# Performance work log

Hardware: AMD Instinct MI355X
Metric: run time of the kernel (lower is better)

The kernel has to match this reference:

```python
import jax, jax.numpy as jnp
import numpy as np

H, KD, VD = 12, 64, 64  # num_heads, k_dim, v_dim
EPS = 1e-12

def _l2norm(x, axis):
    n = jnp.linalg.norm(x, axis=axis, keepdims=True)
    return x / jnp.maximum(n, EPS)

def setup_inputs() -> dict:
    key = jax.random.key(0)
    ks = jax.random.split(key, 6)
    d1, d2 = 768, 768
    return {
        "x1": jax.random.normal(ks[0], (2048, d1), jnp.float32),
        "x2": jax.random.normal(ks[1], (8192, d2), jnp.float32),
        "Wq": jax.random.normal(ks[2], (H * KD, d1), jnp.float32) * 0.03,
        "Wk": jax.random.normal(ks[3], (H * KD, d2), jnp.float32) * 0.03,
        "Wv": jax.random.normal(ks[4], (H * VD, d2), jnp.float32) * 0.03,
        "Wo": jax.random.normal(ks[5], (d1, H * VD), jnp.float32) * 0.03,
        "invt": 20,
    }

def reference(x1, x2, Wq, Wk, Wv, Wo, invt):
    B1 = x1.shape[0]
    B2 = x2.shape[0]
    # Linear (no bias): y = x @ W.T, then split heads
    q = (x1 @ Wq.T).reshape(B1, H, KD)  # [B1,H,KD]
    k = (x2 @ Wk.T).reshape(B2, H, KD)  # [B2,H,KD]
    v = (x2 @ Wv.T).reshape(B2, H, VD)  # [B2,H,VD]
    # per-head L2 normalization over feature dim (cosine attention)
    q = _l2norm(q, axis=-1)
    k = _l2norm(k, axis=-1)
    attn = jnp.einsum("bhd,nhd->hbn", q, k) * jnp.float32(invt)  # [H,B1,B2]
    attn = jax.nn.softmax(attn, axis=-1)
    out = jnp.einsum("hbn,nhd->bhd", attn, v).reshape(B1, H * VD)
    out = out @ Wo.T  # [B1, in_dim1]
    return _l2norm(out, axis=1)
```

## Files before the change

kernel.cpp:

```cpp
#include <hip/hip_runtime.h>
#include <hip/hip_bf16.h>
#include <math.h>

#define B1 2048
#define B2 8192
#define NH 12
#define DH 64
#define DMODEL 768

typedef __attribute__((ext_vector_type(8))) short short8;
typedef __attribute__((ext_vector_type(4))) float floatx4;
typedef __attribute__((ext_vector_type(8))) unsigned short ushort8;
typedef __attribute__((ext_vector_type(4))) unsigned short ushort4v;

static __device__ __forceinline__ unsigned short f2bf(float f) {
  __bf16 b = (__bf16)f;
  return __builtin_bit_cast(unsigned short, b);
}

static __device__ __forceinline__ void gload16(const unsigned short* g,
                                               unsigned short* l) {
  __builtin_amdgcn_global_load_lds(
      (const __attribute__((address_space(1))) void*)g,
      (__attribute__((address_space(3))) void*)l, 16, 0, 0);
}

template <bool L2N, bool F32OUT>
static __device__ __forceinline__ void gemm_tile_f32(
    const float* __restrict__ Ag, const float* __restrict__ Bg,
    void* __restrict__ Cv, int M, int N, int K, int m0, int n0,
    unsigned short* sAh, unsigned short* sBh) {
  const int tid = threadIdx.x;
  const int wave = tid >> 6;
  const int lane = tid & 63;
  const int wm = wave >> 1;
  const int wn = wave & 1;
  const int n15 = lane & 15;
  const int quad = lane >> 4;
  const int srow = lane >> 2;
  const int cpl = (lane & 3) ^ (srow >> 2);

  floatx4 acc[4][4];
#pragma unroll
  for (int i = 0; i < 4; ++i)
#pragma unroll
    for (int j = 0; j < 4; ++j) acc[i][j] = (floatx4){0.f, 0.f, 0.f, 0.f};

  float4 ar[2][2], br[2][2];
#pragma unroll
  for (int jj = 0; jj < 2; ++jj) {
    const int row = (wave * 2 + jj) * 16 + srow;
    const size_t ga = (size_t)(m0 + row) * K + cpl * 8;
    const size_t gb = (size_t)(n0 + row) * K + cpl * 8;
    ar[jj][0] = *(const float4*)&Ag[ga];
    ar[jj][1] = *(const float4*)&Ag[ga + 4];
    br[jj][0] = *(const float4*)&Bg[gb];
    br[jj][1] = *(const float4*)&Bg[gb + 4];
  }

  for (int k0 = 0; k0 < K; k0 += 32) {
    __syncthreads();
#pragma unroll
    for (int jj = 0; jj < 2; ++jj) {
      const int j = wave * 2 + jj;
      const float4 a0 = ar[jj][0], a1 = ar[jj][1];
      const float4 b0 = br[jj][0], b1 = br[jj][1];
      ushort8 ah = {f2bf(a0.x), f2bf(a0.y), f2bf(a0.z), f2bf(a0.w),
                    f2bf(a1.x), f2bf(a1.y), f2bf(a1.z), f2bf(a1.w)};
      ushort8 bh = {f2bf(b0.x), f2bf(b0.y), f2bf(b0.z), f2bf(b0.w),
                    f2bf(b1.x), f2bf(b1.y), f2bf(b1.z), f2bf(b1.w)};
      *(ushort8*)&sAh[j * 512 + lane * 8] = ah;
      *(ushort8*)&sBh[j * 512 + lane * 8] = bh;
    }
    if (k0 + 32 < K) {
#pragma unroll
      for (int jj = 0; jj < 2; ++jj) {
        const int row = (wave * 2 + jj) * 16 + srow;
        const size_t ga = (size_t)(m0 + row) * K + (k0 + 32) + cpl * 8;
        const size_t gb = (size_t)(n0 + row) * K + (k0 + 32) + cpl * 8;
        ar[jj][0] = *(const float4*)&Ag[ga];
        ar[jj][1] = *(const float4*)&Ag[ga + 4];
        br[jj][0] = *(const float4*)&Bg[gb];
        br[jj][1] = *(const float4*)&Bg[gb + 4];
      }
    }
    __syncthreads();

    short8 afh[4];
#pragma unroll
    for (int mt = 0; mt < 4; ++mt) {
      const int row = wm * 64 + mt * 16 + n15;
      const int off = row * 32 + ((quad ^ (n15 >> 2)) << 3);
      afh[mt] = *(const short8*)&sAh[off];
    }
#pragma unroll
    for (int nt = 0; nt < 4; ++nt) {
      const int row = wn * 64 + nt * 16 + n15;
      const int off = row * 32 + ((quad ^ (n15 >> 2)) << 3);
      const short8 bfh = *(const short8*)&sBh[off];
#pragma unroll
      for (int mt = 0; mt < 4; ++mt)
        acc[mt][nt] = __builtin_amdgcn_mfma_f32_16x16x32_bf16(afh[mt], bfh, acc[mt][nt], 0, 0, 0);
    }
  }

#pragma unroll
  for (int mt = 0; mt < 4; ++mt) {
    float scalev[4] = {1.f, 1.f, 1.f, 1.f};
    if constexpr (L2N) {
#pragma unroll
      for (int rr = 0; rr < 4; ++rr) {
        float ss = 0.f;
#pragma unroll
        for (int nt = 0; nt < 4; ++nt) ss += acc[mt][nt][rr] * acc[mt][nt][rr];
        ss += __shfl_xor(ss, 1, 64);
        ss += __shfl_xor(ss, 2, 64);
        ss += __shfl_xor(ss, 4, 64);
        ss += __shfl_xor(ss, 8, 64);
        scalev[rr] = 1.0f / fmaxf(sqrtf(ss), 1e-12f);
      }
    }
#pragma unroll
    for (int nt = 0; nt < 4; ++nt) {
#pragma unroll
      for (int rr = 0; rr < 4; ++rr) {
        const int row = m0 + wm * 64 + mt * 16 + quad * 4 + rr;
        const int col = n0 + wn * 64 + nt * 16 + n15;
        const float v = acc[mt][nt][rr] * scalev[rr];
        if constexpr (F32OUT)
          ((float*)Cv)[(size_t)row * N + col] = v;
        else
          ((unsigned short*)Cv)[(size_t)row * N + col] = f2bf(v);
      }
    }
  }
}

__global__ __launch_bounds__(256) void qkv_proj(
    const float* __restrict__ x1, const float* __restrict__ Wq,
    const float* __restrict__ x2, const float* __restrict__ Wk,
    const float* __restrict__ Wv,
    unsigned short* __restrict__ qbf, unsigned short* __restrict__ kbf,
    unsigned short* __restrict__ vtbf) {
  __shared__ __align__(16) unsigned short sAh[4096], sBh[4096];
  const int bi = blockIdx.x;
  if (bi < 96) {
    gemm_tile_f32<true, false>(x1, Wq, qbf, B1, DMODEL, DMODEL,
                               (bi / 6) * 128, (bi % 6) * 128, sAh, sBh);
  } else if (bi < 480) {
    const int b = bi - 96;
    gemm_tile_f32<true, false>(x2, Wk, kbf, B2, DMODEL, DMODEL,
                               (b / 6) * 128, (b % 6) * 128, sAh, sBh);
  } else {
    const int b = bi - 480;
    gemm_tile_f32<false, false>(Wv, x2, vtbf, DMODEL, B2, DMODEL,
                                (b / 64) * 128, (b % 64) * 128, sAh, sBh);
  }
}

#define KC 128
#define KSPLIT 2
#define NCH (B2 / KSPLIT / KC)
#define PSTR 68

__global__ __launch_bounds__(256, 3) void attn_mfma(
    const unsigned short* __restrict__ qb, const unsigned short* __restrict__ kb,
    const unsigned short* __restrict__ vt, float* __restrict__ aoacc,
    float* __restrict__ lacc, const int* __restrict__ invt_p) {
  __shared__ __align__(16) unsigned short smem[25088];
  unsigned short* Psl = smem + 16384;

  const int bid = blockIdx.x;
  const int swz = (bid & 7) * 96 + (bid >> 3);
  const int zz = swz / 384;
  const int rem = swz - zz * 384;
  const int h = rem >> 5;
  const int q0 = (rem & 31) * 64;

  const float c2 = (float)invt_p[0] * 1.4426950408889634f;
  const int tid = threadIdx.x;
  const int wave = tid >> 6;
  const int lane = tid & 63;
  const int qsub = wave >> 1;
  const int ksub = wave & 1;
  const int n15 = lane & 15;
  const int quad = lane >> 4;
  const int kz0 = zz * (B2 / KSPLIT);

  unsigned short* Ps = &Psl[wave * 32 * PSTR];

  short8 qf[2][2];
#pragma unroll
  for (int qt = 0; qt < 2; ++qt)
#pragma unroll
    for (int ks = 0; ks < 2; ++ks) {
      const int qrow = q0 + qsub * 32 + qt * 16 + n15;
      qf[qt][ks] = *(const short8*)&qb[(size_t)qrow * DMODEL + h * DH + ks * 32 + quad * 8];
    }

  floatx4 oacc[2][4];
#pragma unroll
  for (int qt = 0; qt < 2; ++qt)
#pragma unroll
    for (int nt = 0; nt < 4; ++nt) oacc[qt][nt] = (floatx4){0.f, 0.f, 0.f, 0.f};
  float lsum[2] = {0.f, 0.f};

  const unsigned short* kbp = kb + (size_t)kz0 * DMODEL + h * DH;
  const unsigned short* vbp = vt + (size_t)(h * DH) * B2 + kz0;

  ushort8 kr[4];
#pragma unroll
  for (int i = 0; i < 4; ++i) {
    const int s = i * 256 + tid;
    const int key = s >> 3, cpk = s & 7, chk = cpk ^ (key & 7);
    kr[i] = *(const ushort8*)&kbp[(size_t)key * DMODEL + chk * 8];
  }
#pragma unroll
  for (int i = 0; i < 4; ++i) {
    const int s = i * 256 + tid;
    const int key = s >> 3, cpk = s & 7;
    *(ushort8*)&smem[key * 64 + cpk * 8] = kr[i];
  }
#pragma unroll
  for (int i = 0; i < 4; ++i) {
    const int s = i * 256 + tid;
    const int key = s >> 3, cpk = s & 7, chk = cpk ^ (key & 7);
    kr[i] = *(const ushort8*)&kbp[(size_t)(KC + key) * DMODEL + chk * 8];
  }
  __syncthreads();

  for (int c = 0; c < NCH; ++c) {
    unsigned short* Kb = &smem[(c & 1) * 8192];
    unsigned short* Kn = &smem[((c + 1) & 1) * 8192];
    const unsigned short* vc_ = vbp + c * KC;

    ushort8 vr[8];
#pragma unroll
    for (int ks = 0; ks < 2; ++ks)
#pragma unroll
      for (int nt = 0; nt < 4; ++nt)
        vr[ks * 4 + nt] = *(const ushort8*)&vc_[
            (size_t)(nt * 16 + n15) * B2 + (ksub * 8 + ks * 4 + quad) * 8];

    if (c + 1 < NCH) {
#pragma unroll
      for (int i = 0; i < 4; ++i) {
        const int s = i * 256 + tid;
        const int key = s >> 3, cpk = s & 7;
        *(ushort8*)&Kn[key * 64 + cpk * 8] = kr[i];
      }
      if (c + 2 < NCH) {
        const unsigned short* k2 = kbp + (size_t)(c + 2) * KC * DMODEL;
#pragma unroll
        for (int i = 0; i < 4; ++i) {
          const int s = i * 256 + tid;
          const int key = s >> 3, cpk = s & 7, chk = cpk ^ (key & 7);
          kr[i] = *(const ushort8*)&k2[(size_t)key * DMODEL + chk * 8];
        }
      }
    }

#pragma unroll
    for (int kt = 0; kt < 4; ++kt) {
      floatx4 s0 = {0.f, 0.f, 0.f, 0.f}, s1 = {0.f, 0.f, 0.f, 0.f};
#pragma unroll
      for (int ks = 0; ks < 2; ++ks) {
        const int key = ksub * 64 + kt * 16 + n15;
        const int cp = (ks * 4 + quad) ^ (n15 & 7);
        const short8 kf = *(const short8*)&Kb[key * 64 + cp * 8];
        s0 = __builtin_amdgcn_mfma_f32_16x16x32_bf16(kf, qf[0][ks], s0, 0, 0, 0);
        s1 = __builtin_amdgcn_mfma_f32_16x16x32_bf16(kf, qf[1][ks], s1, 0, 0, 0);
      }
      ushort4v p0, p1;
#pragma unroll
      for (int r = 0; r < 4; ++r) {
        const float e0 = exp2f(fmaf(s0[r], c2, -c2));
        const float e1 = exp2f(fmaf(s1[r], c2, -c2));
        lsum[0] += e0;
        lsum[1] += e1;
        p0[r] = f2bf(e0);
        p1[r] = f2bf(e1);
      }
      *(ushort4v*)&Ps[(0 * 16 + n15) * PSTR + kt * 16 + quad * 4] = p0;
      *(ushort4v*)&Ps[(1 * 16 + n15) * PSTR + kt * 16 + quad * 4] = p1;
    }

#pragma unroll
    for (int ks = 0; ks < 2; ++ks) {
      short8 pa[2];
#pragma unroll
      for (int qt = 0; qt < 2; ++qt)
        pa[qt] = *(const short8*)&Ps[(qt * 16 + n15) * PSTR + ks * 32 + quad * 8];
#pragma unroll
      for (int nt = 0; nt < 4; ++nt) {
        const short8 vf = __builtin_bit_cast(short8, vr[ks * 4 + nt]);
        oacc[0][nt] = __builtin_amdgcn_mfma_f32_16x16x32_bf16(pa[0], vf, oacc[0][nt], 0, 0, 0);
        oacc[1][nt] = __builtin_amdgcn_mfma_f32_16x16x32_bf16(pa[1], vf, oacc[1][nt], 0, 0, 0);
      }
    }

    __syncthreads();
  }

#pragma unroll
  for (int qt = 0; qt < 2; ++qt) {
    float v = lsum[qt];
    v += __shfl_xor(v, 16, 64);
    v += __shfl_xor(v, 32, 64);
    lsum[qt] = v;
  }

  float* aoz = aoacc + (size_t)zz * B1 * DMODEL;
  float* lz = lacc + (size_t)zz * B1 * NH;

  __syncthreads();
  float* Osc = (float*)smem;
  float* lsc = Osc + 4096;
  if (ksub == 1) {
#pragma unroll
    for (int qt = 0; qt < 2; ++qt)
#pragma unroll
      for (int nt = 0; nt < 4; ++nt)
#pragma unroll
        for (int r = 0; r < 4; ++r) {
          const int row = qsub * 32 + qt * 16 + quad * 4 + r;
          Osc[row * 64 + nt * 16 + n15] = oacc[qt][nt][r];
        }
    if (quad == 0) {
      lsc[qsub * 32 + n15] = lsum[0];
      lsc[qsub * 32 + 16 + n15] = lsum[1];
    }
  }
  __syncthreads();
  if (ksub == 0) {
#pragma unroll
    for (int qt = 0; qt < 2; ++qt)
#pragma unroll
      for (int nt = 0; nt < 4; ++nt)
#pragma unroll
        for (int r = 0; r < 4; ++r) {
          const int row = qsub * 32 + qt * 16 + quad * 4 + r;
          const float v = oacc[qt][nt][r] + Osc[row * 64 + nt * 16 + n15];
          aoz[(size_t)(q0 + row) * DMODEL + h * DH + nt * 16 + n15] = v;
        }
    if (quad == 0) {
      lz[(size_t)(q0 + qsub * 32 + n15) * NH + h] = lsum[0] + lsc[qsub * 32 + n15];
      lz[(size_t)(q0 + qsub * 32 + 16 + n15) * NH + h] =
          lsum[1] + lsc[qsub * 32 + 16 + n15];
    }
  }
}

__global__ __launch_bounds__(256) void wo_proj(
    const float* __restrict__ aoacc, const float* __restrict__ lacc,
    const float* __restrict__ Wo, float* __restrict__ woout) {
  __shared__ __align__(16) unsigned short sAh[4096], sBh[4096];
  const int bi = blockIdx.x;
  const int m0 = (bi / 6) * 128;
  const int n0 = (bi % 6) * 128;
  const int tid = threadIdx.x;
  const int wave = tid >> 6;
  const int lane = tid & 63;
  const int wm = wave >> 1;
  const int wn = wave & 1;
  const int n15 = lane & 15;
  const int quad = lane >> 4;
  const int srow = lane >> 2;
  const int cpl = (lane & 3) ^ (srow >> 2);

  const float* ao1 = aoacc + (size_t)B1 * DMODEL;
  const float* la1 = lacc + (size_t)B1 * NH;

  floatx4 acc[4][4];
#pragma unroll
  for (int i = 0; i < 4; ++i)
#pragma unroll
    for (int j = 0; j < 4; ++j) acc[i][j] = (floatx4){0.f, 0.f, 0.f, 0.f};

  for (int k0 = 0; k0 < DMODEL; k0 += 32) {
    __syncthreads();
#pragma unroll
    for (int jj = 0; jj < 2; ++jj) {
      const int j = wave * 2 + jj;
      const int row = j * 16 + srow;
      const size_t ga = (size_t)(m0 + row) * DMODEL + k0 + cpl * 8;
      const float4 a0 = *(const float4*)&aoacc[ga];
      const float4 a1 = *(const float4*)&aoacc[ga + 4];
      const float4 b0 = *(const float4*)&ao1[ga];
      const float4 b1 = *(const float4*)&ao1[ga + 4];
      const int head = (k0 + cpl * 8) >> 6;
      const float lsum = lacc[(m0 + row) * NH + head] + la1[(m0 + row) * NH + head];
      const float inv = 1.0f / lsum;
      ushort8 ah = {f2bf((a0.x + b0.x) * inv), f2bf((a0.y + b0.y) * inv),
                    f2bf((a0.z + b0.z) * inv), f2bf((a0.w + b0.w) * inv),
                    f2bf((a1.x + b1.x) * inv), f2bf((a1.y + b1.y) * inv),
                    f2bf((a1.z + b1.z) * inv), f2bf((a1.w + b1.w) * inv)};
      *(ushort8*)&sAh[j * 512 + lane * 8] = ah;
      const size_t gb = (size_t)(n0 + row) * DMODEL + k0 + cpl * 8;
      const float4 w0 = *(const float4*)&Wo[gb];
      const float4 w1 = *(const float4*)&Wo[gb + 4];
      ushort8 bh = {f2bf(w0.x), f2bf(w0.y), f2bf(w0.z), f2bf(w0.w),
                    f2bf(w1.x), f2bf(w1.y), f2bf(w1.z), f2bf(w1.w)};
      *(ushort8*)&sBh[j * 512 + lane * 8] = bh;
    }
    __syncthreads();

    short8 afh[4];
#pragma unroll
    for (int mt = 0; mt < 4; ++mt) {
      const int row = wm * 64 + mt * 16 + n15;
      afh[mt] = *(const short8*)&sAh[row * 32 + ((quad ^ (n15 >> 2)) << 3)];
    }
#pragma unroll
    for (int nt = 0; nt < 4; ++nt) {
      const int row = wn * 64 + nt * 16 + n15;
      const short8 bfh = *(const short8*)&sBh[row * 32 + ((quad ^ (n15 >> 2)) << 3)];
#pragma unroll
      for (int mt = 0; mt < 4; ++mt)
        acc[mt][nt] = __builtin_amdgcn_mfma_f32_16x16x32_bf16(afh[mt], bfh, acc[mt][nt], 0, 0, 0);
    }
  }

#pragma unroll
  for (int mt = 0; mt < 4; ++mt)
#pragma unroll
    for (int nt = 0; nt < 4; ++nt)
#pragma unroll
      for (int rr = 0; rr < 4; ++rr) {
        const int row = m0 + wm * 64 + mt * 16 + quad * 4 + rr;
        const int col = n0 + wn * 64 + nt * 16 + n15;
        woout[(size_t)row * DMODEL + col] = acc[mt][nt][rr];
      }
}

__global__ __launch_bounds__(256) void l2norm_rows768_out(
    const float* __restrict__ x, float* __restrict__ out) {
  const int row = blockIdx.x;
  const float* xr = &x[(size_t)row * DMODEL];
  float ss = 0.0f;
  float vals[3];
#pragma unroll
  for (int i = 0; i < 3; ++i) {
    vals[i] = xr[threadIdx.x + i * 256];
    ss += vals[i] * vals[i];
  }
#pragma unroll
  for (int off = 32; off > 0; off >>= 1) ss += __shfl_xor(ss, off, 64);
  __shared__ float ws[4];
  if ((threadIdx.x & 63) == 0) ws[threadIdx.x >> 6] = ss;
  __syncthreads();
  const float tot = ws[0] + ws[1] + ws[2] + ws[3];
  const float sc = 1.0f / fmaxf(sqrtf(tot), 1e-12f);
  float* orow = &out[(size_t)row * DMODEL];
#pragma unroll
  for (int i = 0; i < 3; ++i) orow[threadIdx.x + i * 256] = vals[i] * sc;
}

extern "C" void kernel_launch(void* const* d_in, const int* in_sizes, int n_in,
                              void* d_out, int out_size, void* d_ws,
                              size_t ws_size, hipStream_t stream) {
  const float* x1 = (const float*)d_in[0];
  const float* x2 = (const float*)d_in[1];
  const float* Wq = (const float*)d_in[2];
  const float* Wk = (const float*)d_in[3];
  const float* Wv = (const float*)d_in[4];
  const float* Wo = (const float*)d_in[5];
  const int* invt = (const int*)d_in[6];
  float* outp = (float*)d_out;

  char* ws = (char*)d_ws;
  float* aoacc = (float*)(ws + 0);
  float* woout = (float*)(ws + 12582912);
  unsigned short* vt_bf = (unsigned short*)(ws + 18874368);
  float* lacc = (float*)(ws + 32636928);
  unsigned short* q_bf = (unsigned short*)(ws + 38535168);
  unsigned short* k_bf = (unsigned short*)(ws + 41680896);

  qkv_proj<<<864, 256, 0, stream>>>(x1, Wq, x2, Wk, Wv, q_bf, k_bf, vt_bf);
  attn_mfma<<<768, 256, 0, stream>>>(q_bf, k_bf, vt_bf, aoacc, lacc, invt);
  wo_proj<<<96, 256, 0, stream>>>(aoacc, lacc, Wo, woout);
  l2norm_rows768_out<<<B1, 256, 0, stream>>>(woout, outp);
}
```

Measured before the change: 291.1 us.

## Split-K the output projection and double-buffer LDS in the projection GEMMs

```diff
diff --git a/kernel.cpp b/kernel.cpp
--- a/kernel.cpp
+++ b/kernel.cpp
@@ -18,18 +18,11 @@
   return __builtin_bit_cast(unsigned short, b);
 }
 
-static __device__ __forceinline__ void gload16(const unsigned short* g,
-                                               unsigned short* l) {
-  __builtin_amdgcn_global_load_lds(
-      (const __attribute__((address_space(1))) void*)g,
-      (__attribute__((address_space(3))) void*)l, 16, 0, 0);
-}
-
 template <bool L2N, bool F32OUT>
 static __device__ __forceinline__ void gemm_tile_f32(
     const float* __restrict__ Ag, const float* __restrict__ Bg,
     void* __restrict__ Cv, int M, int N, int K, int m0, int n0,
-    unsigned short* sAh, unsigned short* sBh) {
+    unsigned short* sA, unsigned short* sB) {
   const int tid = threadIdx.x;
   const int wave = tid >> 6;
   const int lane = tid & 63;
@@ -39,6 +32,7 @@
   const int quad = lane >> 4;
   const int srow = lane >> 2;
   const int cpl = (lane & 3) ^ (srow >> 2);
+  const int nstep = K >> 5;
 
   floatx4 acc[4][4];
 #pragma unroll
@@ -57,51 +51,77 @@
     br[jj][0] = *(const float4*)&Bg[gb];
     br[jj][1] = *(const float4*)&Bg[gb + 4];
   }
-
-  for (int k0 = 0; k0 < K; k0 += 32) {
-    __syncthreads();
+#pragma unroll
+  for (int jj = 0; jj < 2; ++jj) {
+    const int j = wave * 2 + jj;
+    const float4 a0 = ar[jj][0], a1 = ar[jj][1];
+    const float4 b0 = br[jj][0], b1 = br[jj][1];
+    ushort8 ah = {f2bf(a0.x), f2bf(a0.y), f2bf(a0.z), f2bf(a0.w),
+                  f2bf(a1.x), f2bf(a1.y), f2bf(a1.z), f2bf(a1.w)};
+    ushort8 bh = {f2bf(b0.x), f2bf(b0.y), f2bf(b0.z), f2bf(b0.w),
+                  f2bf(b1.x), f2bf(b1.y), f2bf(b1.z), f2bf(b1.w)};
+    *(ushort8*)&sA[j * 512 + lane * 8] = ah;
+    *(ushort8*)&sB[j * 512 + lane * 8] = bh;
+  }
+  if (nstep > 1) {
 #pragma unroll
     for (int jj = 0; jj < 2; ++jj) {
-      const int j = wave * 2 + jj;
-      const float4 a0 = ar[jj][0], a1 = ar[jj][1];
-      const float4 b0 = br[jj][0], b1 = br[jj][1];
-      ushort8 ah = {f2bf(a0.x), f2bf(a0.y), f2bf(a0.z), f2bf(a0.w),
-                    f2bf(a1.x), f2bf(a1.y), f2bf(a1.z), f2bf(a1.w)};
-      ushort8 bh = {f2bf(b0.x), f2bf(b0.y), f2bf(b0.z), f2bf(b0.w),
-                    f2bf(b1.x), f2bf(b1.y), f2bf(b1.z), f2bf(b1.w)};
-      *(ushort8*)&sAh[j * 512 + lane * 8] = ah;
-      *(ushort8*)&sBh[j * 512 + lane * 8] = bh;
-    }
-    if (k0 + 32 < K) {
+      const int row = (wave * 2 + jj) * 16 + srow;
+      const size_t ga = (size_t)(m0 + row) * K + 32 + cpl * 8;
+      const size_t gb = (size_t)(n0 + row) * K + 32 + cpl * 8;
+      ar[jj][0] = *(const float4*)&Ag[ga];
+      ar[jj][1] = *(const float4*)&Ag[ga + 4];
+      br[jj][0] = *(const float4*)&Bg[gb];
+      br[jj][1] = *(const float4*)&Bg[gb + 4];
+    }
+  }
+  __syncthreads();
+
+  for (int k = 0; k < nstep; ++k) {
+    const int cb = (k & 1) * 4096;
+    if (k + 1 < nstep) {
+      const int nb = ((k + 1) & 1) * 4096;
 #pragma unroll
       for (int jj = 0; jj < 2; ++jj) {
-        const int row = (wave * 2 + jj) * 16 + srow;
-        const size_t ga = (size_t)(m0 + row) * K + (k0 + 32) + cpl * 8;
-        const size_t gb = (size_t)(n0 + row) * K + (k0 + 32) + cpl * 8;
-        ar[jj][0] = *(const float4*)&Ag[ga];
-        ar[jj][1] = *(const float4*)&Ag[ga + 4];
-        br[jj][0] = *(const float4*)&Bg[gb];
-        br[jj][1] = *(const float4*)&Bg[gb + 4];
-      }
-    }
-    __syncthreads();
+        const int j = wave * 2 + jj;
+        const float4 a0 = ar[jj][0], a1 = ar[jj][1];
+        const float4 b0 = br[jj][0], b1 = br[jj][1];
+        ushort8 ah = {f2bf(a0.x), f2bf(a0.y), f2bf(a0.z), f2bf(a0.w),
+                      f2bf(a1.x), f2bf(a1.y), f2bf(a1.z), f2bf(a1.w)};
+        ushort8 bh = {f2bf(b0.x), f2bf(b0.y), f2bf(b0.z), f2bf(b0.w),
+                      f2bf(b1.x), f2bf(b1.y), f2bf(b1.z), f2bf(b1.w)};
+        *(ushort8*)&sA[nb + j * 512 + lane * 8] = ah;
+        *(ushort8*)&sB[nb + j * 512 + lane * 8] = bh;
+      }
+      if (k + 2 < nstep) {
+#pragma unroll
+        for (int jj = 0; jj < 2; ++jj) {
+          const int row = (wave * 2 + jj) * 16 + srow;
+          const size_t ga = (size_t)(m0 + row) * K + (k + 2) * 32 + cpl * 8;
+          const size_t gb = (size_t)(n0 + row) * K + (k + 2) * 32 + cpl * 8;
+          ar[jj][0] = *(const float4*)&Ag[ga];
+          ar[jj][1] = *(const float4*)&Ag[ga + 4];
+          br[jj][0] = *(const float4*)&Bg[gb];
+          br[jj][1] = *(const float4*)&Bg[gb + 4];
+        }
+      }
+    }
 
     short8 afh[4];
 #pragma unroll
     for (int mt = 0; mt < 4; ++mt) {
       const int row = wm * 64 + mt * 16 + n15;
-      const int off = row * 32 + ((quad ^ (n15 >> 2)) << 3);
-      afh[mt] = *(const short8*)&sAh[off];
+      afh[mt] = *(const short8*)&sA[cb + row * 32 + ((quad ^ (n15 >> 2)) << 3)];
     }
 #pragma unroll
     for (int nt = 0; nt < 4; ++nt) {
       const int row = wn * 64 + nt * 16 + n15;
-      const int off = row * 32 + ((quad ^ (n15 >> 2)) << 3);
-      const short8 bfh = *(const short8*)&sBh[off];
+      const short8 bfh = *(const short8*)&sB[cb + row * 32 + ((quad ^ (n15 >> 2)) << 3)];
 #pragma unroll
       for (int mt = 0; mt < 4; ++mt)
         acc[mt][nt] = __builtin_amdgcn_mfma_f32_16x16x32_bf16(afh[mt], bfh, acc[mt][nt], 0, 0, 0);
     }
+    __syncthreads();
   }
 
 #pragma unroll
@@ -142,19 +162,19 @@
     const float* __restrict__ Wv,
     unsigned short* __restrict__ qbf, unsigned short* __restrict__ kbf,
     unsigned short* __restrict__ vtbf) {
-  __shared__ __align__(16) unsigned short sAh[4096], sBh[4096];
+  __shared__ __align__(16) unsigned short sA[8192], sB[8192];
   const int bi = blockIdx.x;
   if (bi < 96) {
     gemm_tile_f32<true, false>(x1, Wq, qbf, B1, DMODEL, DMODEL,
-                               (bi / 6) * 128, (bi % 6) * 128, sAh, sBh);
+                               (bi / 6) * 128, (bi % 6) * 128, sA, sB);
   } else if (bi < 480) {
     const int b = bi - 96;
     gemm_tile_f32<true, false>(x2, Wk, kbf, B2, DMODEL, DMODEL,
-                               (b / 6) * 128, (b % 6) * 128, sAh, sBh);
+                               (b / 6) * 128, (b % 6) * 128, sA, sB);
   } else {
     const int b = bi - 480;
     gemm_tile_f32<false, false>(Wv, x2, vtbf, DMODEL, B2, DMODEL,
-                                (b / 64) * 128, (b % 64) * 128, sAh, sBh);
+                                (b / 64) * 128, (b % 64) * 128, sA, sB);
   }
 }
 
@@ -354,10 +374,14 @@
 __global__ __launch_bounds__(256) void wo_proj(
     const float* __restrict__ aoacc, const float* __restrict__ lacc,
     const float* __restrict__ Wo, float* __restrict__ woout) {
-  __shared__ __align__(16) unsigned short sAh[4096], sBh[4096];
-  const int bi = blockIdx.x;
-  const int m0 = (bi / 6) * 128;
-  const int n0 = (bi % 6) * 128;
+  __shared__ __align__(16) unsigned short sA[8192], sB[8192];
+  const int bid = blockIdx.x;
+  const int t = bid % 96;
+  const int kz = bid / 96;
+  const int m0 = (t / 6) * 128;
+  const int n0 = (t % 6) * 128;
+  const int kbase = kz * 256;
+  const int nstep = 8;
   const int tid = threadIdx.x;
   const int wave = tid >> 6;
   const int lane = tid & 63;
@@ -377,50 +401,78 @@
 #pragma unroll
     for (int j = 0; j < 4; ++j) acc[i][j] = (floatx4){0.f, 0.f, 0.f, 0.f};
 
-  for (int k0 = 0; k0 < DMODEL; k0 += 32) {
-    __syncthreads();
-#pragma unroll
-    for (int jj = 0; jj < 2; ++jj) {
-      const int j = wave * 2 + jj;
-      const int row = j * 16 + srow;
-      const size_t ga = (size_t)(m0 + row) * DMODEL + k0 + cpl * 8;
-      const float4 a0 = *(const float4*)&aoacc[ga];
-      const float4 a1 = *(const float4*)&aoacc[ga + 4];
-      const float4 b0 = *(const float4*)&ao1[ga];
-      const float4 b1 = *(const float4*)&ao1[ga + 4];
-      const int head = (k0 + cpl * 8) >> 6;
-      const float lsum = lacc[(m0 + row) * NH + head] + la1[(m0 + row) * NH + head];
-      const float inv = 1.0f / lsum;
-      ushort8 ah = {f2bf((a0.x + b0.x) * inv), f2bf((a0.y + b0.y) * inv),
-                    f2bf((a0.z + b0.z) * inv), f2bf((a0.w + b0.w) * inv),
-                    f2bf((a1.x + b1.x) * inv), f2bf((a1.y + b1.y) * inv),
-                    f2bf((a1.z + b1.z) * inv), f2bf((a1.w + b1.w) * inv)};
-      *(ushort8*)&sAh[j * 512 + lane * 8] = ah;
-      const size_t gb = (size_t)(n0 + row) * DMODEL + k0 + cpl * 8;
-      const float4 w0 = *(const float4*)&Wo[gb];
-      const float4 w1 = *(const float4*)&Wo[gb + 4];
-      ushort8 bh = {f2bf(w0.x), f2bf(w0.y), f2bf(w0.z), f2bf(w0.w),
-                    f2bf(w1.x), f2bf(w1.y), f2bf(w1.z), f2bf(w1.w)};
-      *(ushort8*)&sBh[j * 512 + lane * 8] = bh;
-    }
-    __syncthreads();
+  float4 Aa[2][2], Ab[2][2], Bw[2][2];
+  float lw[2];
+
+#define WO_LOADSTEP(s)                                                        \
+  {                                                                           \
+    const int kk = kbase + (s) * 32;                                          \
+    _Pragma("unroll") for (int jj = 0; jj < 2; ++jj) {                        \
+      const int row = (wave * 2 + jj) * 16 + srow;                            \
+      const size_t ga = (size_t)(m0 + row) * DMODEL + kk + cpl * 8;           \
+      const size_t gb = (size_t)(n0 + row) * DMODEL + kk + cpl * 8;           \
+      Aa[jj][0] = *(const float4*)&aoacc[ga];                                 \
+      Aa[jj][1] = *(const float4*)&aoacc[ga + 4];                             \
+      Ab[jj][0] = *(const float4*)&ao1[ga];                                   \
+      Ab[jj][1] = *(const float4*)&ao1[ga + 4];                               \
+      Bw[jj][0] = *(const float4*)&Wo[gb];                                    \
+      Bw[jj][1] = *(const float4*)&Wo[gb + 4];                                \
+      const int head = (kk + cpl * 8) >> 6;                                   \
+      const int li = (m0 + row) * NH + head;                                  \
+      lw[jj] = lacc[li] + la1[li];                                            \
+    }                                                                         \
+  }
+
+#define WO_WRITEBUF(boff)                                                     \
+  {                                                                           \
+    _Pragma("unroll") for (int jj = 0; jj < 2; ++jj) {                        \
+      const int j = wave * 2 + jj;                                            \
+      const float inv = 1.0f / lw[jj];                                        \
+      const float4 a0 = Aa[jj][0], a1 = Aa[jj][1];                            \
+      const float4 b0 = Ab[jj][0], b1 = Ab[jj][1];                            \
+      const float4 w0 = Bw[jj][0], w1 = Bw[jj][1];                            \
+      ushort8 ah = {f2bf((a0.x + b0.x) * inv), f2bf((a0.y + b0.y) * inv),     \
+                    f2bf((a0.z + b0.z) * inv), f2bf((a0.w + b0.w) * inv),     \
+                    f2bf((a1.x + b1.x) * inv), f2bf((a1.y + b1.y) * inv),     \
+                    f2bf((a1.z + b1.z) * inv), f2bf((a1.w + b1.w) * inv)};    \
+      ushort8 bh = {f2bf(w0.x), f2bf(w0.y), f2bf(w0.z), f2bf(w0.w),           \
+                    f2bf(w1.x), f2bf(w1.y), f2bf(w1.z), f2bf(w1.w)};          \
+      *(ushort8*)&sA[(boff) + j * 512 + lane * 8] = ah;                       \
+      *(ushort8*)&sB[(boff) + j * 512 + lane * 8] = bh;                       \
+    }                                                                         \
+  }
+
+  WO_LOADSTEP(0);
+  WO_WRITEBUF(0);
+  WO_LOADSTEP(1);
+  __syncthreads();
+
+  for (int k = 0; k < nstep; ++k) {
+    const int cb = (k & 1) * 4096;
+    if (k + 1 < nstep) {
+      const int nb = ((k + 1) & 1) * 4096;
+      WO_WRITEBUF(nb);
+      if (k + 2 < nstep) WO_LOADSTEP(k + 2);
+    }
 
     short8 afh[4];
 #pragma unroll
     for (int mt = 0; mt < 4; ++mt) {
       const int row = wm * 64 + mt * 16 + n15;
-      afh[mt] = *(const short8*)&sAh[row * 32 + ((quad ^ (n15 >> 2)) << 3)];
+      afh[mt] = *(const short8*)&sA[cb + row * 32 + ((quad ^ (n15 >> 2)) << 3)];
     }
 #pragma unroll
     for (int nt = 0; nt < 4; ++nt) {
       const int row = wn * 64 + nt * 16 + n15;
-      const short8 bfh = *(const short8*)&sBh[row * 32 + ((quad ^ (n15 >> 2)) << 3)];
+      const short8 bfh = *(const short8*)&sB[cb + row * 32 + ((quad ^ (n15 >> 2)) << 3)];
 #pragma unroll
       for (int mt = 0; mt < 4; ++mt)
         acc[mt][nt] = __builtin_amdgcn_mfma_f32_16x16x32_bf16(afh[mt], bfh, acc[mt][nt], 0, 0, 0);
     }
-  }
-
+    __syncthreads();
+  }
+
+  float* wslab = woout + (size_t)kz * B1 * DMODEL;
 #pragma unroll
   for (int mt = 0; mt < 4; ++mt)
 #pragma unroll
@@ -429,19 +481,24 @@
       for (int rr = 0; rr < 4; ++rr) {
         const int row = m0 + wm * 64 + mt * 16 + quad * 4 + rr;
         const int col = n0 + wn * 64 + nt * 16 + n15;
-        woout[(size_t)row * DMODEL + col] = acc[mt][nt][rr];
-      }
+        wslab[(size_t)row * DMODEL + col] = acc[mt][nt][rr];
+      }
+#undef WO_LOADSTEP
+#undef WO_WRITEBUF
 }
 
 __global__ __launch_bounds__(256) void l2norm_rows768_out(
     const float* __restrict__ x, float* __restrict__ out) {
   const int row = blockIdx.x;
-  const float* xr = &x[(size_t)row * DMODEL];
+  const float* x0 = &x[(size_t)row * DMODEL];
+  const float* x1s = x0 + (size_t)B1 * DMODEL;
+  const float* x2s = x0 + 2 * (size_t)B1 * DMODEL;
   float ss = 0.0f;
   float vals[3];
 #pragma unroll
   for (int i = 0; i < 3; ++i) {
-    vals[i] = xr[threadIdx.x + i * 256];
+    const int c = threadIdx.x + i * 256;
+    vals[i] = x0[c] + x1s[c] + x2s[c];
     ss += vals[i] * vals[i];
   }
 #pragma unroll
@@ -478,6 +535,6 @@
 
   qkv_proj<<<864, 256, 0, stream>>>(x1, Wq, x2, Wk, Wv, q_bf, k_bf, vt_bf);
   attn_mfma<<<768, 256, 0, stream>>>(q_bf, k_bf, vt_bf, aoacc, lacc, invt);
-  wo_proj<<<96, 256, 0, stream>>>(aoacc, lacc, Wo, woout);
+  wo_proj<<<288, 256, 0, stream>>>(aoacc, lacc, Wo, woout);
   l2norm_rows768_out<<<B1, 256, 0, stream>>>(woout, outp);
 }
```

Result: faster. 283.9 us (-2.5%).
